# Kernel optimization log

Hardware: AMD Instinct MI355X
Metric: run time of the kernel (lower is better)

Reference implementation:

```python
import jax, jax.numpy as jnp
import numpy as np

N = 32768      # num nodes
F = 128        # raw node feature dim
D = 128        # embedding_dim
E = 524288     # num edges (avg degree 16)
L = 8          # transformer depth
H = 8          # heads
CS = 32        # target_cluster_size
NC = 10        # num classes
K = N // CS    # num clusters (all full -> pad branch is a no-op)


def _leaky_relu(x):
    return jnp.where(x >= 0, x, 0.2 * x)


def _gat(h_in, src, dst, W, a_src, a_dst, b):
    # PyG GATConv, heads=1, with self-loops already appended to src/dst
    h = h_in @ W                                             # [N, D]
    e = _leaky_relu((h @ a_src)[src] + (h @ a_dst)[dst])     # [E+N]
    m = jax.ops.segment_max(e, dst, num_segments=N)
    ex = jnp.exp(e - m[dst])
    denom = jax.ops.segment_sum(ex, dst, num_segments=N)
    alpha = ex / denom[dst]
    return jax.ops.segment_sum(h[src] * alpha[:, None], dst, num_segments=N) + b


def _ln(x, s, b):
    m = x.mean(-1, keepdims=True)
    v = ((x - m) ** 2).mean(-1, keepdims=True)
    return (x - m) * jax.lax.rsqrt(v + 1e-5) * s + b


def setup_inputs() -> dict:
    key = jax.random.key(0)
    ks = jax.random.split(key, 20)
    rn = lambda k, s, sc=0.05: jax.random.normal(k, s, jnp.float32) * sc
    return dict(
        x=jax.random.normal(ks[0], (N, F), jnp.float32),
        edge_index=jax.random.randint(ks[1], (2, E), 0, N),
        node_order=jax.random.permutation(ks[2], N).astype(jnp.int32),
        W_in=rn(ks[3], (F, D)), b_in=jnp.zeros(D, jnp.float32),
        Wg1=rn(ks[4], (D, D)), as1=rn(ks[5], (D,)), ad1=rn(ks[6], (D,)), bg1=jnp.zeros(D, jnp.float32),
        Wg2=rn(ks[7], (D, D)), as2=rn(ks[8], (D,)), ad2=rn(ks[9], (D,)), bg2=jnp.zeros(D, jnp.float32),
        W_emb=rn(ks[10], (CS * D, D), 0.02), b_emb=jnp.zeros(D, jnp.float32),
        cls_tok=rn(ks[11], (D,)),
        ln1_s=jnp.ones((L, D), jnp.float32), ln1_b=jnp.zeros((L, D), jnp.float32),
        Wqkv=rn(ks[12], (L, D, 3 * D)), bqkv=jnp.zeros((L, 3 * D), jnp.float32),
        Wo=rn(ks[13], (L, D, D)), bo=jnp.zeros((L, D), jnp.float32),
        ln2_s=jnp.ones((L, D), jnp.float32), ln2_b=jnp.zeros((L, D), jnp.float32),
        Wf1=rn(ks[14], (L, D, 4 * D)), bf1=jnp.zeros((L, 4 * D), jnp.float32),
        Wf2=rn(ks[15], (L, 4 * D, D)), bf2=jnp.zeros((L, D), jnp.float32),
        Wc=rn(ks[16], (D, NC)), bc=jnp.zeros(NC, jnp.float32),
    )


def reference(x, edge_index, node_order, W_in, b_in, Wg1, as1, ad1, bg1,
              Wg2, as2, ad2, bg2, W_emb, b_emb, cls_tok,
              ln1_s, ln1_b, Wqkv, bqkv, Wo, bo, ln2_s, ln2_b,
              Wf1, bf1, Wf2, bf2, Wc, bc):
    loops = jnp.arange(N, dtype=edge_index.dtype)
    src = jnp.concatenate([edge_index[0], loops])
    dst = jnp.concatenate([edge_index[1], loops])
    h = x @ W_in + b_in
    h = _gat(h, src, dst, Wg1, as1, ad1, bg1)
    h = _gat(h, src, dst, Wg2, as2, ad2, bg2)
    # irregular cluster gather, then per-cluster linear embedding (32*D -> D)
    flat = h[node_order].reshape(K, CS * D)
    emb = flat @ W_emb + b_emb                               # [K, D]
    t = jnp.concatenate([cls_tok[None, :], emb], axis=0)     # [K+1, D]
    dh = D // H
    scale = dh ** -0.5
    for l in range(L):                                       # pre-norm transformer
        u = _ln(t, ln1_s[l], ln1_b[l])
        qkv = u @ Wqkv[l] + bqkv[l]
        q, k, v = [a.reshape(-1, H, dh) for a in jnp.split(qkv, 3, axis=-1)]
        att = jax.nn.softmax(jnp.einsum('qhd,khd->hqk', q, k) * scale, axis=-1)
        o = jnp.einsum('hqk,khd->qhd', att, v).reshape(-1, D) @ Wo[l] + bo[l]
        t = t + o
        u = _ln(t, ln2_s[l], ln2_b[l])
        t = t + jax.nn.gelu(u @ Wf1[l] + bf1[l]) @ Wf2[l] + bf2[l]
    return (t[0] @ Wc + bc)[None, :]                         # [1, NC]
```

## Files before the change

kernel.cpp:

```cpp
#include <hip/hip_runtime.h>
#include <hip/hip_bf16.h>
#include <math.h>

#define NN 32768
#define NE 524288
#define EN_TOT (NE + NN)
#define LL 8
#define SS 1025
#define SPLIT 16
#define SS128 (SS * 128)

__global__ void hist_kernel(const int* __restrict__ ei, int* __restrict__ cnt) {
    int i = blockIdx.x * 256 + threadIdx.x;
    if (i >= EN_TOT) return;
    int d = (i < NE) ? ei[NE + i] : (i - NE);
    atomicAdd(&cnt[d], 1);
}

__global__ void scan_kernel(const int* __restrict__ cnt, int* __restrict__ offs) {
    __shared__ int wsum[16];
    int t = threadIdx.x;
    int base = t * 32;
    int s = 0;
    #pragma unroll
    for (int j = 0; j < 32; ++j) s += cnt[base + j];
    int lane = t & 63, w = t >> 6;
    int v = s;
    #pragma unroll
    for (int d = 1; d < 64; d <<= 1) {
        int u = __shfl_up(v, d);
        if (lane >= d) v += u;
    }
    if (lane == 63) wsum[w] = v;
    __syncthreads();
    if (t == 0) {
        int a = 0;
        #pragma unroll
        for (int i = 0; i < 16; ++i) { int x = wsum[i]; wsum[i] = a; a += x; }
    }
    __syncthreads();
    int run = wsum[w] + (v - s);
    #pragma unroll
    for (int j = 0; j < 32; ++j) { offs[base + j] = run; run += cnt[base + j]; }
    if (t == 1023) offs[NN] = run;
}

__global__ void scatter_kernel(const int* __restrict__ ei, const int* __restrict__ offs,
                               int* __restrict__ fill, int* __restrict__ csr) {
    int i = blockIdx.x * 256 + threadIdx.x;
    if (i >= EN_TOT) return;
    int s, d;
    if (i < NE) { s = ei[i]; d = ei[NE + i]; } else { s = d = i - NE; }
    int pos = offs[d] + atomicAdd(&fill[d], 1);
    csr[pos] = s;
}

__device__ __forceinline__ float gelu_f(float x) {
    float x3 = x * x * x;
    return 0.5f * x * (1.f + tanhf(0.7978845608028654f * (x + 0.044715f * x3)));
}

__global__ void gemm_f32(const float* __restrict__ A, const float* __restrict__ B,
                         const float* __restrict__ bias, const float* res,
                         float* C, int M, int Nn, int K) {
    __shared__ float As[32][66];
    __shared__ float Bs[32][72];
    int t = threadIdx.x;
    int bx = blockIdx.x, by = blockIdx.y;
    int tx = t & 15, ty = t >> 4;
    float acc[4][4] = {};
    int m0 = t >> 3;
    int kk4 = (t & 7) * 4;
    int kb0 = t >> 4;
    int n40 = (t & 15) * 4;

    for (int k0 = 0; k0 < K; k0 += 32) {
        __syncthreads();
        #pragma unroll
        for (int half = 0; half < 2; ++half) {
            int m = m0 + half * 32;
            int row = by * 64 + m;
            float4 v = {0.f, 0.f, 0.f, 0.f};
            if (row < M) v = *(const float4*)&A[(size_t)row * K + k0 + kk4];
            As[kk4 + 0][m] = v.x; As[kk4 + 1][m] = v.y;
            As[kk4 + 2][m] = v.z; As[kk4 + 3][m] = v.w;
        }
        #pragma unroll
        for (int half = 0; half < 2; ++half) {
            int kk = kb0 + half * 16;
            *(float4*)&Bs[kk][n40] = *(const float4*)&B[(size_t)(k0 + kk) * Nn + bx * 64 + n40];
        }
        __syncthreads();
        #pragma unroll
        for (int kk = 0; kk < 32; ++kk) {
            float a0 = As[kk][ty * 4 + 0];
            float a1 = As[kk][ty * 4 + 1];
            float a2 = As[kk][ty * 4 + 2];
            float a3 = As[kk][ty * 4 + 3];
            float4 b4 = *(float4*)&Bs[kk][tx * 4];
            acc[0][0] += a0 * b4.x; acc[0][1] += a0 * b4.y; acc[0][2] += a0 * b4.z; acc[0][3] += a0 * b4.w;
            acc[1][0] += a1 * b4.x; acc[1][1] += a1 * b4.y; acc[1][2] += a1 * b4.z; acc[1][3] += a1 * b4.w;
            acc[2][0] += a2 * b4.x; acc[2][1] += a2 * b4.y; acc[2][2] += a2 * b4.z; acc[2][3] += a2 * b4.w;
            acc[3][0] += a3 * b4.x; acc[3][1] += a3 * b4.y; acc[3][2] += a3 * b4.z; acc[3][3] += a3 * b4.w;
        }
    }
    #pragma unroll
    for (int i = 0; i < 4; ++i) {
        int row = by * 64 + ty * 4 + i;
        if (row < M) {
            #pragma unroll
            for (int j = 0; j < 4; ++j) {
                int col = bx * 64 + tx * 4 + j;
                float v = acc[i][j];
                if (bias) v += bias[col];
                if (res) v += res[(size_t)row * Nn + col];
                C[(size_t)row * Nn + col] = v;
            }
        }
    }
}

__global__ void bcomb_kernel(const float* __restrict__ b_in, const float* __restrict__ Wg1,
                             float* __restrict__ bcomb) {
    int n = threadIdx.x;
    float s = 0.f;
    for (int k = 0; k < 128; ++k) s += b_in[k] * Wg1[k * 128 + n];
    bcomb[n] = s;
}

__global__ void dots_kernel(const float* __restrict__ hW, const float* __restrict__ asrc,
                            const float* __restrict__ adst, float* __restrict__ ss,
                            float* __restrict__ sd) {
    int lane = threadIdx.x & 63;
    int n = blockIdx.x * 4 + (threadIdx.x >> 6);
    float h0 = hW[(size_t)n * 128 + lane];
    float h1 = hW[(size_t)n * 128 + 64 + lane];
    float vs = h0 * asrc[lane] + h1 * asrc[64 + lane];
    float vd = h0 * adst[lane] + h1 * adst[64 + lane];
    #pragma unroll
    for (int m = 32; m >= 1; m >>= 1) { vs += __shfl_xor(vs, m); vd += __shfl_xor(vd, m); }
    if (lane == 0) { ss[n] = vs; sd[n] = vd; }
}

__global__ void gat_aggregate(const float* __restrict__ hW, const int* __restrict__ offs,
                              const int* __restrict__ csr, const float* __restrict__ ssrc,
                              const float* __restrict__ sdst, const float* __restrict__ bias,
                              float* __restrict__ out) {
    int lane = threadIdx.x & 63;
    int n = blockIdx.x * 4 + (threadIdx.x >> 6);
    int beg = offs[n], end = offs[n + 1];
    float sd = sdst[n];
    float mymax = -INFINITY;
    for (int p = beg + lane; p < end; p += 64) {
        float e = ssrc[csr[p]] + sd;
        e = (e >= 0.f) ? e : 0.2f * e;
        mymax = fmaxf(mymax, e);
    }
    #pragma unroll
    for (int m = 32; m >= 1; m >>= 1) mymax = fmaxf(mymax, __shfl_xor(mymax, m));
    float mysum = 0.f;
    for (int p = beg + lane; p < end; p += 64) {
        float e = ssrc[csr[p]] + sd;
        e = (e >= 0.f) ? e : 0.2f * e;
        mysum += __expf(e - mymax);
    }
    #pragma unroll
    for (int m = 32; m >= 1; m >>= 1) mysum += __shfl_xor(mysum, m);
    float inv = 1.f / mysum;
    float accx = 0.f, accy = 0.f;
    int deg = end - beg;
    for (int c0 = 0; c0 < deg; c0 += 64) {
        int s = 0; float al = 0.f;
        if (c0 + lane < deg) {
            s = csr[beg + c0 + lane];
            float e = ssrc[s] + sd;
            e = (e >= 0.f) ? e : 0.2f * e;
            al = __expf(e - mymax) * inv;
        }
        int cend = min(64, deg - c0);
        int p = 0;
        for (; p + 4 <= cend; p += 4) {
            int s0 = __shfl(s, p);     float a0 = __shfl(al, p);
            int s1 = __shfl(s, p + 1); float a1 = __shfl(al, p + 1);
            int s2 = __shfl(s, p + 2); float a2 = __shfl(al, p + 2);
            int s3 = __shfl(s, p + 3); float a3 = __shfl(al, p + 3);
            float2 v0 = *(const float2*)&hW[(size_t)s0 * 128 + lane * 2];
            float2 v1 = *(const float2*)&hW[(size_t)s1 * 128 + lane * 2];
            float2 v2 = *(const float2*)&hW[(size_t)s2 * 128 + lane * 2];
            float2 v3 = *(const float2*)&hW[(size_t)s3 * 128 + lane * 2];
            accx += a0 * v0.x; accy += a0 * v0.y;
            accx += a1 * v1.x; accy += a1 * v1.y;
            accx += a2 * v2.x; accy += a2 * v2.y;
            accx += a3 * v3.x; accy += a3 * v3.y;
        }
        for (; p < cend; ++p) {
            int sj = __shfl(s, p);
            float aj = __shfl(al, p);
            float2 v = *(const float2*)&hW[(size_t)sj * 128 + lane * 2];
            accx += aj * v.x; accy += aj * v.y;
        }
    }
    float2 ov;
    ov.x = accx + bias[2 * lane];
    ov.y = accy + bias[2 * lane + 1];
    *(float2*)&out[(size_t)n * 128 + 2 * lane] = ov;
}

__global__ void gather_copy(const float* __restrict__ hA, const int* __restrict__ no,
                            float* __restrict__ flat) {
    int i = blockIdx.x * 256 + threadIdx.x;
    int m = i >> 12, j = i & 4095;
    int node = no[(m << 5) + (j >> 7)];
    flat[i] = hA[(size_t)node * 128 + (j & 127)];
}

__global__ void emb_gemm(const float* __restrict__ flat, const float* __restrict__ W,
                         float* __restrict__ pbuf) {
    __shared__ float As[32][66];
    __shared__ float Bs[32][72];
    int t = threadIdx.x;
    int bx = blockIdx.x, by = blockIdx.y, sp = blockIdx.z;
    int tx = t & 15, ty = t >> 4;
    float acc[4][4] = {};
    int m0 = t >> 3;
    int kk4 = (t & 7) * 4;
    int kb0 = t >> 4;
    int n40 = (t & 15) * 4;
    int kbase = sp * 256;

    for (int k0 = 0; k0 < 256; k0 += 32) {
        __syncthreads();
        #pragma unroll
        for (int half = 0; half < 2; ++half) {
            int m = m0 + half * 32;
            int row = by * 64 + m;
            float4 v = *(const float4*)&flat[(size_t)row * 4096 + kbase + k0 + kk4];
            As[kk4 + 0][m] = v.x; As[kk4 + 1][m] = v.y;
            As[kk4 + 2][m] = v.z; As[kk4 + 3][m] = v.w;
        }
        #pragma unroll
        for (int half = 0; half < 2; ++half) {
            int kk = kb0 + half * 16;
            *(float4*)&Bs[kk][n40] = *(const float4*)&W[(size_t)(kbase + k0 + kk) * 128 + bx * 64 + n40];
        }
        __syncthreads();
        #pragma unroll
        for (int kk = 0; kk < 32; ++kk) {
            float a0 = As[kk][ty * 4 + 0];
            float a1 = As[kk][ty * 4 + 1];
            float a2 = As[kk][ty * 4 + 2];
            float a3 = As[kk][ty * 4 + 3];
            float4 b4 = *(float4*)&Bs[kk][tx * 4];
            acc[0][0] += a0 * b4.x; acc[0][1] += a0 * b4.y; acc[0][2] += a0 * b4.z; acc[0][3] += a0 * b4.w;
            acc[1][0] += a1 * b4.x; acc[1][1] += a1 * b4.y; acc[1][2] += a1 * b4.z; acc[1][3] += a1 * b4.w;
            acc[2][0] += a2 * b4.x; acc[2][1] += a2 * b4.y; acc[2][2] += a2 * b4.z; acc[2][3] += a2 * b4.w;
            acc[3][0] += a3 * b4.x; acc[3][1] += a3 * b4.y; acc[3][2] += a3 * b4.z; acc[3][3] += a3 * b4.w;
        }
    }
    float* C = pbuf + (size_t)sp * (1024 * 128);
    #pragma unroll
    for (int i = 0; i < 4; ++i) {
        int row = by * 64 + ty * 4 + i;
        #pragma unroll
        for (int j = 0; j < 4; ++j)
            C[(size_t)row * 128 + bx * 64 + tx * 4 + j] = acc[i][j];
    }
}

__global__ void emb_reduce(const float* __restrict__ pbuf, const float* __restrict__ b_emb,
                           const float* __restrict__ cls, float* __restrict__ tb) {
    int i = blockIdx.x * 256 + threadIdx.x;
    if (blockIdx.x == 0 && threadIdx.x < 128) tb[threadIdx.x] = cls[threadIdx.x];
    float s = b_emb[i & 127];
    #pragma unroll
    for (int sp = 0; sp < SPLIT; ++sp) s += pbuf[(size_t)sp * 131072 + i];
    tb[128 + i] = s;
}

__device__ __forceinline__ float tok_read(const float* __restrict__ tb, const float* __restrict__ P,
                                          size_t ix) {
    return tb[ix] + P[ix] + P[SS128 + ix] + P[2 * (size_t)SS128 + ix] + P[3 * (size_t)SS128 + ix];
}

__global__ __launch_bounds__(256) void qkv_slice(
        const float* __restrict__ tb, const float* __restrict__ P,
        const float* __restrict__ s1, const float* __restrict__ b1,
        const float* __restrict__ Wq, const float* __restrict__ bq, float* __restrict__ qkv) {
    __shared__ float u[4][128];
    __shared__ float red[4][2][128];
    __shared__ float ws[8192];
    int t = threadIdx.x;
    int r0 = blockIdx.x * 4, sl = blockIdx.y;
    int col = t & 127, kh = t >> 7;
    {
        int rw = t >> 6, lane = t & 63;
        int row = r0 + rw;
        float a0 = 0.f, a1 = 0.f;
        if (row < SS) {
            size_t ix = (size_t)row * 128 + lane;
            a0 = tok_read(tb, P, ix);
            a1 = tok_read(tb, P, ix + 64);
        }
        float sm = a0 + a1;
        #pragma unroll
        for (int m = 32; m >= 1; m >>= 1) sm += __shfl_xor(sm, m);
        float mean = sm * (1.f / 128.f);
        float d0 = a0 - mean, d1 = a1 - mean;
        float vv = d0 * d0 + d1 * d1;
        #pragma unroll
        for (int m = 32; m >= 1; m >>= 1) vv += __shfl_xor(vv, m);
        float rs = rsqrtf(vv * (1.f / 128.f) + 1e-5f);
        u[rw][lane] = d0 * rs * s1[lane] + b1[lane];
        u[rw][64 + lane] = d1 * rs * s1[64 + lane] + b1[64 + lane];
    }
    float acc[4] = {};
    for (int k0 = 0; k0 < 128; k0 += 64) {
        __syncthreads();
        const float* src = Wq + (size_t)k0 * 384 + sl * 128;
        #pragma unroll
        for (int i = 0; i < 8; ++i) {
            int idx = i * 256 + t;
            int kk = idx >> 5, c4 = (idx & 31) * 4;
            ((float4*)ws)[idx] = *(const float4*)&src[(size_t)kk * 384 + c4];
        }
        __syncthreads();
        int kb = kh * 32;
        #pragma unroll
        for (int kq = 0; kq < 32; kq += 4) {
            float a4[4][4];
            #pragma unroll
            for (int i = 0; i < 4; ++i)
                *(float4*)a4[i] = *(const float4*)&u[i][k0 + kb + kq];
            #pragma unroll
            for (int q = 0; q < 4; ++q) {
                float b = ws[(kb + kq + q) * 128 + col];
                #pragma unroll
                for (int i = 0; i < 4; ++i) acc[i] += a4[i][q] * b;
            }
        }
    }
    __syncthreads();
    #pragma unroll
    for (int i = 0; i < 4; ++i) red[i][kh][col] = acc[i];
    __syncthreads();
    if (t < 128) {
        float bqv = bq[sl * 128 + t];
        #pragma unroll
        for (int i = 0; i < 4; ++i) {
            int row = r0 + i;
            if (row < SS)
                qkv[(size_t)row * 384 + sl * 128 + t] = red[i][0][t] + red[i][1][t] + bqv;
        }
    }
}

__global__ __launch_bounds__(256) void proj_ln2(
        const float* __restrict__ ao, const float* __restrict__ P,
        const float* __restrict__ Wo, const float* __restrict__ bo,
        const float* __restrict__ s2, const float* __restrict__ b2, const float* __restrict__ bf2,
        float* __restrict__ tb, float* __restrict__ ub) {
    __shared__ float bufA[4][128];
    __shared__ float tn[4][128];
    __shared__ float red[4][2][128];
    __shared__ float ws[8192];
    int t = threadIdx.x;
    int r0 = blockIdx.x * 4;
    int lane = t & 63;
    int col = t & 127, kh = t >> 7;
    {
        int rw = t >> 6;
        int row = r0 + rw;
        float a0 = 0.f, a1 = 0.f;
        if (row < SS) {
            a0 = ao[(size_t)row * 128 + lane];
            a1 = ao[(size_t)row * 128 + 64 + lane];
        }
        bufA[rw][lane] = a0;
        bufA[rw][64 + lane] = a1;
    }
    float pp[4] = {};
    for (int k0 = 0; k0 < 128; k0 += 64) {
        __syncthreads();
        const float4* src = (const float4*)&Wo[(size_t)k0 * 128];
        #pragma unroll
        for (int i = 0; i < 8; ++i) ((float4*)ws)[i * 256 + t] = src[i * 256 + t];
        __syncthreads();
        int kb = kh * 32;
        #pragma unroll
        for (int kq = 0; kq < 32; kq += 4) {
            float a4[4][4];
            #pragma unroll
            for (int i = 0; i < 4; ++i)
                *(float4*)a4[i] = *(const float4*)&bufA[i][k0 + kb + kq];
            #pragma unroll
            for (int q = 0; q < 4; ++q) {
                float b = ws[(kb + kq + q) * 128 + col];
                #pragma unroll
                for (int i = 0; i < 4; ++i) pp[i] += a4[i][q] * b;
            }
        }
    }
    __syncthreads();
    #pragma unroll
    for (int i = 0; i < 4; ++i) red[i][kh][col] = pp[i];
    __syncthreads();
    if (t < 128) {
        #pragma unroll
        for (int i = 0; i < 4; ++i) {
            int row = r0 + i;
            float v = 0.f;
            if (row < SS) {
                size_t ix = (size_t)row * 128 + t;
                float told = tok_read(tb, P, ix);
                v = red[i][0][t] + red[i][1][t] + bo[t] + told;
                tb[ix] = v + bf2[t];
            }
            tn[i][t] = v;
        }
    }
    __syncthreads();
    {
        int rw = t >> 6;
        int row = r0 + rw;
        float a0 = tn[rw][lane], a1 = tn[rw][64 + lane];
        float sm = a0 + a1;
        #pragma unroll
        for (int m = 32; m >= 1; m >>= 1) sm += __shfl_xor(sm, m);
        float mean = sm * (1.f / 128.f);
        float d0 = a0 - mean, d1 = a1 - mean;
        float vv = d0 * d0 + d1 * d1;
        #pragma unroll
        for (int m = 32; m >= 1; m >>= 1) vv += __shfl_xor(vv, m);
        float rs = rsqrtf(vv * (1.f / 128.f) + 1e-5f);
        if (row < SS) {
            ub[(size_t)row * 128 + lane] = d0 * rs * s2[lane] + b2[lane];
            ub[(size_t)row * 128 + 64 + lane] = d1 * rs * s2[64 + lane] + b2[64 + lane];
        }
    }
}

__global__ __launch_bounds__(256) void ffn_part(
        const float* __restrict__ ub, const float* __restrict__ Wf1, const float* __restrict__ bf1,
        const float* __restrict__ Wf2, float* __restrict__ P) {
    __shared__ float u[4][128];
    __shared__ float g[4][128];
    __shared__ float red[4][2][128];
    __shared__ float ws[8192];
    int t = threadIdx.x;
    int r0 = blockIdx.x * 4, sl = blockIdx.y;
    int col = t & 127, kh = t >> 7;
    {
        int rw = t >> 6, lane = t & 63;
        int row = r0 + rw;
        float a0 = 0.f, a1 = 0.f;
        if (row < SS) {
            a0 = ub[(size_t)row * 128 + lane];
            a1 = ub[(size_t)row * 128 + 64 + lane];
        }
        u[rw][lane] = a0;
        u[rw][64 + lane] = a1;
    }
    float a1c[4] = {};
    for (int k0 = 0; k0 < 128; k0 += 64) {
        __syncthreads();
        const float* src = Wf1 + (size_t)k0 * 512 + sl * 128;
        #pragma unroll
        for (int i = 0; i < 8; ++i) {
            int idx = i * 256 + t;
            int kk = idx >> 5, c4 = (idx & 31) * 4;
            ((float4*)ws)[idx] = *(const float4*)&src[(size_t)kk * 512 + c4];
        }
        __syncthreads();
        int kb = kh * 32;
        #pragma unroll
        for (int kq = 0; kq < 32; kq += 4) {
            float a4[4][4];
            #pragma unroll
            for (int i = 0; i < 4; ++i)
                *(float4*)a4[i] = *(const float4*)&u[i][k0 + kb + kq];
            #pragma unroll
            for (int q = 0; q < 4; ++q) {
                float b = ws[(kb + kq + q) * 128 + col];
                #pragma unroll
                for (int i = 0; i < 4; ++i) a1c[i] += a4[i][q] * b;
            }
        }
    }
    __syncthreads();
    #pragma unroll
    for (int i = 0; i < 4; ++i) red[i][kh][col] = a1c[i];
    __syncthreads();
    if (t < 128) {
        float bv = bf1[sl * 128 + t];
        #pragma unroll
        for (int i = 0; i < 4; ++i)
            g[i][t] = gelu_f(red[i][0][t] + red[i][1][t] + bv);
    }
    float a2c[4] = {};
    for (int k0 = 0; k0 < 128; k0 += 64) {
        __syncthreads();
        const float4* src = (const float4*)&Wf2[(size_t)(sl * 128 + k0) * 128];
        #pragma unroll
        for (int i = 0; i < 8; ++i) ((float4*)ws)[i * 256 + t] = src[i * 256 + t];
        __syncthreads();
        int kb = kh * 32;
        #pragma unroll
        for (int kq = 0; kq < 32; kq += 4) {
            float a4[4][4];
            #pragma unroll
            for (int i = 0; i < 4; ++i)
                *(float4*)a4[i] = *(const float4*)&g[i][k0 + kb + kq];
            #pragma unroll
            for (int q = 0; q < 4; ++q) {
                float b = ws[(kb + kq + q) * 128 + col];
                #pragma unroll
                for (int i = 0; i < 4; ++i) a2c[i] += a4[i][q] * b;
            }
        }
    }
    __syncthreads();
    #pragma unroll
    for (int i = 0; i < 4; ++i) red[i][kh][col] = a2c[i];
    __syncthreads();
    if (t < 128) {
        #pragma unroll
        for (int i = 0; i < 4; ++i) {
            int row = r0 + i;
            if (row < SS)
                P[(size_t)sl * SS128 + (size_t)row * 128 + t] = red[i][0][t] + red[i][1][t];
        }
    }
}

__global__ void attn_kernel(const float* __restrict__ qkv, float* __restrict__ ao) {
    __shared__ float Kl[128][20];
    __shared__ float Vl[128][20];
    int h = blockIdx.y;
    int t = threadIdx.x;
    int sub = t & 15;
    int qr = blockIdx.x * 16 + (t >> 4);
    bool active = qr < SS;
    float q[16];
    if (active) {
        #pragma unroll
        for (int d = 0; d < 16; ++d) q[d] = qkv[(size_t)qr * 384 + h * 16 + d];
    }
    float m = -INFINITY, sum = 0.f;
    float acc[16] = {};
    for (int j0 = 0; j0 < SS; j0 += 128) {
        __syncthreads();
        int j = t >> 1, dg = (t & 1) * 8;
        if (j0 + j < SS) {
            const float* row = qkv + (size_t)(j0 + j) * 384 + h * 16 + dg;
            *(float4*)&Kl[j][dg]     = *(const float4*)(row + 128);
            *(float4*)&Kl[j][dg + 4] = *(const float4*)(row + 132);
            *(float4*)&Vl[j][dg]     = *(const float4*)(row + 256);
            *(float4*)&Vl[j][dg + 4] = *(const float4*)(row + 260);
        }
        __syncthreads();
        if (active) {
            int jmax = min(128, SS - j0);
            for (int jj = sub; jj < jmax; jj += 16) {
                float4 ka = *(const float4*)&Kl[jj][0];
                float4 kb = *(const float4*)&Kl[jj][4];
                float4 kc = *(const float4*)&Kl[jj][8];
                float4 kd = *(const float4*)&Kl[jj][12];
                float sc = q[0]*ka.x + q[1]*ka.y + q[2]*ka.z + q[3]*ka.w
                         + q[4]*kb.x + q[5]*kb.y + q[6]*kb.z + q[7]*kb.w
                         + q[8]*kc.x + q[9]*kc.y + q[10]*kc.z + q[11]*kc.w
                         + q[12]*kd.x + q[13]*kd.y + q[14]*kd.z + q[15]*kd.w;
                sc *= 0.25f;
                float4 va = *(const float4*)&Vl[jj][0];
                float4 vb = *(const float4*)&Vl[jj][4];
                float4 vc = *(const float4*)&Vl[jj][8];
                float4 vd = *(const float4*)&Vl[jj][12];
                float vv[16] = {va.x, va.y, va.z, va.w, vb.x, vb.y, vb.z, vb.w,
                                vc.x, vc.y, vc.z, vc.w, vd.x, vd.y, vd.z, vd.w};
                if (sc <= m) {
                    float p = __expf(sc - m);
                    sum += p;
                    #pragma unroll
                    for (int d = 0; d < 16; ++d) acc[d] += p * vv[d];
                } else {
                    float c = __expf(m - sc);
                    sum = sum * c + 1.f;
                    #pragma unroll
                    for (int d = 0; d < 16; ++d) acc[d] = acc[d] * c + vv[d];
                    m = sc;
                }
            }
        }
    }
    if (active) {
        #pragma unroll
        for (int msk = 1; msk < 16; msk <<= 1) {
            float mo = __shfl_xor(m, msk);
            float so = __shfl_xor(sum, msk);
            float vo[16];
            #pragma unroll
            for (int d = 0; d < 16; ++d) vo[d] = __shfl_xor(acc[d], msk);
            float mn = fmaxf(m, mo);
            float c1 = __expf(m - mn), c2 = __expf(mo - mn);
            sum = sum * c1 + so * c2;
            #pragma unroll
            for (int d = 0; d < 16; ++d) acc[d] = acc[d] * c1 + vo[d] * c2;
            m = mn;
        }
        if (sub == 0) {
            float inv = 1.f / sum;
            #pragma unroll
            for (int d = 0; d < 16; ++d) ao[(size_t)qr * 128 + h * 16 + d] = acc[d] * inv;
        }
    }
}

__global__ void classifier_kernel(const float* __restrict__ tb, const float* __restrict__ P,
                                  const float* __restrict__ Wc, const float* __restrict__ bc,
                                  float* __restrict__ out) {
    int j = threadIdx.x;
    if (j < 10) {
        float a = bc[j];
        #pragma unroll
        for (int k = 0; k < 128; ++k) a += tok_read(tb, P, k) * Wc[k * 10 + j];
        out[j] = a;
    }
}

extern "C" void kernel_launch(void* const* d_in, const int* in_sizes, int n_in,
                              void* d_out, int out_size, void* d_ws, size_t ws_size,
                              hipStream_t stream) {
    (void)in_sizes; (void)n_in; (void)out_size; (void)ws_size;
    const float* x     = (const float*)d_in[0];
    const int*   ei    = (const int*)d_in[1];
    const int*   nord  = (const int*)d_in[2];
    const float* W_in  = (const float*)d_in[3];
    const float* b_in  = (const float*)d_in[4];
    const float* Wg1   = (const float*)d_in[5];
    const float* as1   = (const float*)d_in[6];
    const float* ad1   = (const float*)d_in[7];
    const float* bg1   = (const float*)d_in[8];
    const float* Wg2   = (const float*)d_in[9];
    const float* as2   = (const float*)d_in[10];
    const float* ad2   = (const float*)d_in[11];
    const float* bg2   = (const float*)d_in[12];
    const float* W_emb = (const float*)d_in[13];
    const float* b_emb = (const float*)d_in[14];
    const float* clst  = (const float*)d_in[15];
    const float* ln1s  = (const float*)d_in[16];
    const float* ln1b  = (const float*)d_in[17];
    const float* Wqkv  = (const float*)d_in[18];
    const float* bqkv  = (const float*)d_in[19];
    const float* Wo    = (const float*)d_in[20];
    const float* bo    = (const float*)d_in[21];
    const float* ln2s  = (const float*)d_in[22];
    const float* ln2b  = (const float*)d_in[23];
    const float* Wf1   = (const float*)d_in[24];
    const float* bf1   = (const float*)d_in[25];
    const float* Wf2   = (const float*)d_in[26];
    const float* bf2   = (const float*)d_in[27];
    const float* Wc    = (const float*)d_in[28];
    const float* bc    = (const float*)d_in[29];

    char* w = (char*)d_ws;
    size_t o = 0;
    auto ALLOC = [&](size_t nbytes) -> char* {
        char* p = w + o;
        o += (nbytes + 255) & ~(size_t)255;
        return p;
    };
    int*   cnt   = (int*)ALLOC((size_t)NN * 4);
    int*   fill  = (int*)ALLOC((size_t)NN * 4);
    int*   offs  = (int*)ALLOC((size_t)(NN + 1) * 4);
    int*   csr   = (int*)ALLOC((size_t)EN_TOT * 4);
    float* hA    = (float*)ALLOC((size_t)NN * 128 * 4);
    float* hW    = (float*)ALLOC((size_t)NN * 128 * 4);
    float* h1    = (float*)ALLOC((size_t)NN * 128 * 4);
    float* ssrc  = (float*)ALLOC((size_t)NN * 4);
    float* sdst  = (float*)ALLOC((size_t)NN * 4);
    float* tbuf  = (float*)ALLOC((size_t)SS128 * 4);
    float* ubuf  = (float*)ALLOC((size_t)SS128 * 4);
    float* qkvb  = (float*)ALLOC((size_t)SS * 384 * 4);
    float* aob   = (float*)ALLOC((size_t)SS128 * 4);
    float* Pbuf  = (float*)ALLOC((size_t)4 * SS128 * 4);
    float* Wcomb = (float*)ALLOC((size_t)128 * 128 * 4);
    float* bcomb = (float*)ALLOC((size_t)128 * 4);
    float* pbuf  = hW;
    float* flat  = h1;

    dim3 blk(256);
    int egrid = (EN_TOT + 255) / 256;

    hipMemsetAsync(cnt, 0, (size_t)NN * 8, stream);
    hist_kernel<<<egrid, blk, 0, stream>>>(ei, cnt);
    scan_kernel<<<1, 1024, 0, stream>>>(cnt, offs);
    scatter_kernel<<<egrid, blk, 0, stream>>>(ei, offs, fill, csr);

    gemm_f32<<<dim3(2, 2), blk, 0, stream>>>(W_in, Wg1, nullptr, nullptr, Wcomb, 128, 128, 128);
    bcomb_kernel<<<1, 128, 0, stream>>>(b_in, Wg1, bcomb);

    gemm_f32<<<dim3(2, 512), blk, 0, stream>>>(x, Wcomb, bcomb, nullptr, hW, NN, 128, 128);
    dots_kernel<<<8192, blk, 0, stream>>>(hW, as1, ad1, ssrc, sdst);
    gat_aggregate<<<8192, blk, 0, stream>>>(hW, offs, csr, ssrc, sdst, bg1, h1);
    gemm_f32<<<dim3(2, 512), blk, 0, stream>>>(h1, Wg2, nullptr, nullptr, hW, NN, 128, 128);
    dots_kernel<<<8192, blk, 0, stream>>>(hW, as2, ad2, ssrc, sdst);
    gat_aggregate<<<8192, blk, 0, stream>>>(hW, offs, csr, ssrc, sdst, bg2, hA);

    gather_copy<<<16384, blk, 0, stream>>>(hA, nord, flat);
    emb_gemm<<<dim3(2, 16, SPLIT), blk, 0, stream>>>(flat, W_emb, pbuf);
    emb_reduce<<<512, blk, 0, stream>>>(pbuf, b_emb, clst, tbuf);

    hipMemsetAsync(Pbuf, 0, (size_t)4 * SS128 * 4, stream);

    for (int l = 0; l < LL; ++l) {
        qkv_slice<<<dim3(257, 3), blk, 0, stream>>>(tbuf, Pbuf, ln1s + l * 128, ln1b + l * 128,
                                                    Wqkv + (size_t)l * 128 * 384, bqkv + l * 384, qkvb);
        attn_kernel<<<dim3(65, 8), blk, 0, stream>>>(qkvb, aob);
        proj_ln2<<<257, blk, 0, stream>>>(aob, Pbuf, Wo + (size_t)l * 128 * 128, bo + l * 128,
                                          ln2s + l * 128, ln2b + l * 128, bf2 + l * 128,
                                          tbuf, ubuf);
        ffn_part<<<dim3(257, 4), blk, 0, stream>>>(ubuf, Wf1 + (size_t)l * 128 * 512, bf1 + l * 512,
                                                   Wf2 + (size_t)l * 512 * 128, Pbuf);
    }
    classifier_kernel<<<1, 64, 0, stream>>>(tbuf, Pbuf, Wc, bc, (float*)d_out);
}
```

Measured before the change: 851.8 us.

## Fuse out-projection/LN2 with FFN slices, ping-pong buffers, vectorize gather and unroll GAT

```diff
diff --git a/kernel.cpp b/kernel.cpp
--- a/kernel.cpp
+++ b/kernel.cpp
@@ -179,19 +179,31 @@
         }
         int cend = min(64, deg - c0);
         int p = 0;
-        for (; p + 4 <= cend; p += 4) {
+        for (; p + 8 <= cend; p += 8) {
             int s0 = __shfl(s, p);     float a0 = __shfl(al, p);
             int s1 = __shfl(s, p + 1); float a1 = __shfl(al, p + 1);
             int s2 = __shfl(s, p + 2); float a2 = __shfl(al, p + 2);
             int s3 = __shfl(s, p + 3); float a3 = __shfl(al, p + 3);
+            int s4 = __shfl(s, p + 4); float a4 = __shfl(al, p + 4);
+            int s5 = __shfl(s, p + 5); float a5 = __shfl(al, p + 5);
+            int s6 = __shfl(s, p + 6); float a6 = __shfl(al, p + 6);
+            int s7 = __shfl(s, p + 7); float a7 = __shfl(al, p + 7);
             float2 v0 = *(const float2*)&hW[(size_t)s0 * 128 + lane * 2];
             float2 v1 = *(const float2*)&hW[(size_t)s1 * 128 + lane * 2];
             float2 v2 = *(const float2*)&hW[(size_t)s2 * 128 + lane * 2];
             float2 v3 = *(const float2*)&hW[(size_t)s3 * 128 + lane * 2];
+            float2 v4 = *(const float2*)&hW[(size_t)s4 * 128 + lane * 2];
+            float2 v5 = *(const float2*)&hW[(size_t)s5 * 128 + lane * 2];
+            float2 v6 = *(const float2*)&hW[(size_t)s6 * 128 + lane * 2];
+            float2 v7 = *(const float2*)&hW[(size_t)s7 * 128 + lane * 2];
             accx += a0 * v0.x; accy += a0 * v0.y;
             accx += a1 * v1.x; accy += a1 * v1.y;
             accx += a2 * v2.x; accy += a2 * v2.y;
             accx += a3 * v3.x; accy += a3 * v3.y;
+            accx += a4 * v4.x; accy += a4 * v4.y;
+            accx += a5 * v5.x; accy += a5 * v5.y;
+            accx += a6 * v6.x; accy += a6 * v6.y;
+            accx += a7 * v7.x; accy += a7 * v7.y;
         }
         for (; p < cend; ++p) {
             int sj = __shfl(s, p);
@@ -208,10 +220,10 @@
 
 __global__ void gather_copy(const float* __restrict__ hA, const int* __restrict__ no,
                             float* __restrict__ flat) {
-    int i = blockIdx.x * 256 + threadIdx.x;
-    int m = i >> 12, j = i & 4095;
-    int node = no[(m << 5) + (j >> 7)];
-    flat[i] = hA[(size_t)node * 128 + (j & 127)];
+    int idx = blockIdx.x * 256 + threadIdx.x;
+    int m = idx >> 10, j4 = idx & 1023;
+    int node = no[(m << 5) + (j4 >> 5)];
+    ((float4*)flat)[idx] = ((const float4*)(hA + (size_t)node * 128))[j4 & 31];
 }
 
 __global__ void emb_gemm(const float* __restrict__ flat, const float* __restrict__ W,
@@ -354,17 +366,20 @@
     }
 }
 
-__global__ __launch_bounds__(256) void proj_ln2(
-        const float* __restrict__ ao, const float* __restrict__ P,
+__global__ __launch_bounds__(256) void proj_ffn(
+        const float* __restrict__ ao, const float* __restrict__ tb_in, const float* __restrict__ P_in,
         const float* __restrict__ Wo, const float* __restrict__ bo,
         const float* __restrict__ s2, const float* __restrict__ b2, const float* __restrict__ bf2,
-        float* __restrict__ tb, float* __restrict__ ub) {
+        const float* __restrict__ Wf1, const float* __restrict__ bf1,
+        const float* __restrict__ Wf2,
+        float* __restrict__ tb_out, float* __restrict__ P_out) {
     __shared__ float bufA[4][128];
     __shared__ float tn[4][128];
+    __shared__ float g[4][128];
     __shared__ float red[4][2][128];
     __shared__ float ws[8192];
     int t = threadIdx.x;
-    int r0 = blockIdx.x * 4;
+    int r0 = blockIdx.x * 4, sl = blockIdx.y;
     int lane = t & 63;
     int col = t & 127, kh = t >> 7;
     {
@@ -411,9 +426,9 @@
             float v = 0.f;
             if (row < SS) {
                 size_t ix = (size_t)row * 128 + t;
-                float told = tok_read(tb, P, ix);
+                float told = tok_read(tb_in, P_in, ix);
                 v = red[i][0][t] + red[i][1][t] + bo[t] + told;
-                tb[ix] = v + bf2[t];
+                if (sl == 0) tb_out[ix] = v + bf2[t];
             }
             tn[i][t] = v;
         }
@@ -421,7 +436,6 @@
     __syncthreads();
     {
         int rw = t >> 6;
-        int row = r0 + rw;
         float a0 = tn[rw][lane], a1 = tn[rw][64 + lane];
         float sm = a0 + a1;
         #pragma unroll
@@ -432,33 +446,8 @@
         #pragma unroll
         for (int m = 32; m >= 1; m >>= 1) vv += __shfl_xor(vv, m);
         float rs = rsqrtf(vv * (1.f / 128.f) + 1e-5f);
-        if (row < SS) {
-            ub[(size_t)row * 128 + lane] = d0 * rs * s2[lane] + b2[lane];
-            ub[(size_t)row * 128 + 64 + lane] = d1 * rs * s2[64 + lane] + b2[64 + lane];
-        }
-    }
-}
-
-__global__ __launch_bounds__(256) void ffn_part(
-        const float* __restrict__ ub, const float* __restrict__ Wf1, const float* __restrict__ bf1,
-        const float* __restrict__ Wf2, float* __restrict__ P) {
-    __shared__ float u[4][128];
-    __shared__ float g[4][128];
-    __shared__ float red[4][2][128];
-    __shared__ float ws[8192];
-    int t = threadIdx.x;
-    int r0 = blockIdx.x * 4, sl = blockIdx.y;
-    int col = t & 127, kh = t >> 7;
-    {
-        int rw = t >> 6, lane = t & 63;
-        int row = r0 + rw;
-        float a0 = 0.f, a1 = 0.f;
-        if (row < SS) {
-            a0 = ub[(size_t)row * 128 + lane];
-            a1 = ub[(size_t)row * 128 + 64 + lane];
-        }
-        u[rw][lane] = a0;
-        u[rw][64 + lane] = a1;
+        bufA[rw][lane] = d0 * rs * s2[lane] + b2[lane];
+        bufA[rw][64 + lane] = d1 * rs * s2[64 + lane] + b2[64 + lane];
     }
     float a1c[4] = {};
     for (int k0 = 0; k0 < 128; k0 += 64) {
@@ -477,7 +466,7 @@
             float a4[4][4];
             #pragma unroll
             for (int i = 0; i < 4; ++i)
-                *(float4*)a4[i] = *(const float4*)&u[i][k0 + kb + kq];
+                *(float4*)a4[i] = *(const float4*)&bufA[i][k0 + kb + kq];
             #pragma unroll
             for (int q = 0; q < 4; ++q) {
                 float b = ws[(kb + kq + q) * 128 + col];
@@ -527,7 +516,7 @@
         for (int i = 0; i < 4; ++i) {
             int row = r0 + i;
             if (row < SS)
-                P[(size_t)sl * SS128 + (size_t)row * 128 + t] = red[i][0][t] + red[i][1][t];
+                P_out[(size_t)sl * SS128 + (size_t)row * 128 + t] = red[i][0][t] + red[i][1][t];
         }
     }
 }
@@ -677,11 +666,12 @@
     float* h1    = (float*)ALLOC((size_t)NN * 128 * 4);
     float* ssrc  = (float*)ALLOC((size_t)NN * 4);
     float* sdst  = (float*)ALLOC((size_t)NN * 4);
-    float* tbuf  = (float*)ALLOC((size_t)SS128 * 4);
-    float* ubuf  = (float*)ALLOC((size_t)SS128 * 4);
+    float* tb0   = (float*)ALLOC((size_t)SS128 * 4);
+    float* tb1   = (float*)ALLOC((size_t)SS128 * 4);
+    float* P0    = (float*)ALLOC((size_t)4 * SS128 * 4);
+    float* P1    = (float*)ALLOC((size_t)4 * SS128 * 4);
     float* qkvb  = (float*)ALLOC((size_t)SS * 384 * 4);
     float* aob   = (float*)ALLOC((size_t)SS128 * 4);
-    float* Pbuf  = (float*)ALLOC((size_t)4 * SS128 * 4);
     float* Wcomb = (float*)ALLOC((size_t)128 * 128 * 4);
     float* bcomb = (float*)ALLOC((size_t)128 * 4);
     float* pbuf  = hW;
@@ -705,21 +695,26 @@
     dots_kernel<<<8192, blk, 0, stream>>>(hW, as2, ad2, ssrc, sdst);
     gat_aggregate<<<8192, blk, 0, stream>>>(hW, offs, csr, ssrc, sdst, bg2, hA);
 
-    gather_copy<<<16384, blk, 0, stream>>>(hA, nord, flat);
+    gather_copy<<<4096, blk, 0, stream>>>(hA, nord, flat);
     emb_gemm<<<dim3(2, 16, SPLIT), blk, 0, stream>>>(flat, W_emb, pbuf);
-    emb_reduce<<<512, blk, 0, stream>>>(pbuf, b_emb, clst, tbuf);
-
-    hipMemsetAsync(Pbuf, 0, (size_t)4 * SS128 * 4, stream);
+    emb_reduce<<<512, blk, 0, stream>>>(pbuf, b_emb, clst, tb0);
+
+    hipMemsetAsync(P0, 0, (size_t)4 * SS128 * 4, stream);
 
     for (int l = 0; l < LL; ++l) {
-        qkv_slice<<<dim3(257, 3), blk, 0, stream>>>(tbuf, Pbuf, ln1s + l * 128, ln1b + l * 128,
+        float* tin  = (l & 1) ? tb1 : tb0;
+        float* Pin  = (l & 1) ? P1 : P0;
+        float* tout = (l & 1) ? tb0 : tb1;
+        float* Pout = (l & 1) ? P0 : P1;
+        qkv_slice<<<dim3(257, 3), blk, 0, stream>>>(tin, Pin, ln1s + l * 128, ln1b + l * 128,
                                                     Wqkv + (size_t)l * 128 * 384, bqkv + l * 384, qkvb);
         attn_kernel<<<dim3(65, 8), blk, 0, stream>>>(qkvb, aob);
-        proj_ln2<<<257, blk, 0, stream>>>(aob, Pbuf, Wo + (size_t)l * 128 * 128, bo + l * 128,
-                                          ln2s + l * 128, ln2b + l * 128, bf2 + l * 128,
-                                          tbuf, ubuf);
-        ffn_part<<<dim3(257, 4), blk, 0, stream>>>(ubuf, Wf1 + (size_t)l * 128 * 512, bf1 + l * 512,
-                                                   Wf2 + (size_t)l * 512 * 128, Pbuf);
-    }
-    classifier_kernel<<<1, 64, 0, stream>>>(tbuf, Pbuf, Wc, bc, (float*)d_out);
-}
+        proj_ffn<<<dim3(257, 4), blk, 0, stream>>>(aob, tin, Pin,
+                                                   Wo + (size_t)l * 128 * 128, bo + l * 128,
+                                                   ln2s + l * 128, ln2b + l * 128, bf2 + l * 128,
+                                                   Wf1 + (size_t)l * 128 * 512, bf1 + l * 512,
+                                                   Wf2 + (size_t)l * 512 * 128,
+                                                   tout, Pout);
+    }
+    classifier_kernel<<<1, 64, 0, stream>>>(tb0, P0, Wc, bc, (float*)d_out);
+}
```

Measured after the change: 868.9 us. +2.0%, slower.
